# Optimization experiments

Measured on AMD Instinct MI355X. Metric: run time of the kernel, lower is better.

Reference implementation:

```python
import jax, jax.numpy as jnp
import numpy as np

QMIN, QMAX = -128.0, 127.0

@jax.custom_vjp
def ste_round(x):
    return jnp.round(x)

def _ste_fwd(x):
    return jnp.round(x), None

def _ste_bwd(_, g):
    return (g,)

ste_round.defvjp(_ste_fwd, _ste_bwd)

def fake_quant_act(x, scale):
    # Int8 per-tensor fake quant: q = clip(round(x/s)) * s
    return jnp.clip(ste_round(x / scale), QMIN, QMAX) * scale

def fake_quant_weight(w):
    # Int8WeightPerTensorFloat: scale from max-abs statistic
    s = jnp.max(jnp.abs(w)) / QMAX
    return jnp.clip(ste_round(w / s), QMIN, QMAX) * s

def conv2d(x, w, b, pad):
    y = jax.lax.conv_general_dilated(
        x, w, window_strides=(1, 1), padding=[(pad, pad), (pad, pad)],
        dimension_numbers=('NCHW', 'OIHW', 'NCHW'))
    return y + b[None, :, None, None]

def maxpool2(x):
    return jax.lax.reduce_window(
        x, -jnp.inf, jax.lax.max, (1, 1, 2, 2), (1, 1, 2, 2), 'VALID')

def setup_inputs() -> dict:
    key = jax.random.key(0)
    ks = jax.random.split(key, 12)
    def w_init(k, shape, fan_in):
        return jax.random.normal(k, shape, jnp.float32) * (1.0 / np.sqrt(fan_in))
    inp = {
        'x': jax.random.normal(ks[0], (32, 1, 256, 256), jnp.float32),
        'w1': w_init(ks[1], (16, 1, 3, 3), 1 * 9),
        'b1': jax.random.normal(ks[2], (16,), jnp.float32) * 0.01,
        'w2': w_init(ks[3], (32, 16, 3, 3), 16 * 9),
        'b2': jax.random.normal(ks[4], (32,), jnp.float32) * 0.01,
        'w3': w_init(ks[5], (32, 32, 5, 5), 32 * 25),
        'b3': jax.random.normal(ks[6], (32,), jnp.float32) * 0.01,
        'w4': w_init(ks[7], (16, 32, 3, 3), 32 * 9),
        'b4': jax.random.normal(ks[8], (16,), jnp.float32) * 0.01,
        'wc': w_init(ks[9], (10, 16), 16),
        'bc': jax.random.normal(ks[10], (10,), jnp.float32) * 0.01,
        # 11 learned per-tensor activation scales, kept strictly positive
        'act_scales': jax.random.uniform(ks[11], (11,), jnp.float32) * 0.05 + 0.01,
    }
    return inp

def reference(x, w1, b1, w2, b2, w3, b3, w4, b4, wc, bc, act_scales):
    s = act_scales
    x = fake_quant_act(x, s[0])                                  # input_quant
    x = conv2d(x, fake_quant_weight(w1), b1, 0)                  # conv1 (3x3, p0)
    x = fake_quant_act(jax.nn.relu(x), s[1])                     # relu1
    x = fake_quant_act(x, s[2])                                  # quant1
    x = conv2d(x, fake_quant_weight(w2), b2, 1)                  # conv2 (3x3, p1)
    x = fake_quant_act(jax.nn.relu(x), s[3])                     # relu2
    x = fake_quant_act(x, s[4])                                  # quant2
    x = conv2d(x, fake_quant_weight(w3), b3, 2)                  # conv3 (5x5, p2)
    x = fake_quant_act(jax.nn.relu(x), s[5])                     # relu3
    x = fake_quant_act(x, s[6])                                  # quant3
    x = maxpool2(x)                                              # pool1
    x = fake_quant_act(x, s[7])                                  # pool1_quant
    x = conv2d(x, fake_quant_weight(w4), b4, 0)                  # conv4 (3x3, p0)
    x = fake_quant_act(jax.nn.relu(x), s[8])                     # relu4
    x = fake_quant_act(x, s[9])                                  # quant4
    x = jnp.mean(x, axis=(2, 3))                                 # global avg pool -> [B,16]
    x = fake_quant_act(x, s[10])                                 # pool_quant
    return x @ fake_quant_weight(wc).T + bc                      # classifier -> [B,10]
```

## Files before the change

### kernel.cpp

```cpp
#include <hip/hip_runtime.h>
#include <math.h>


typedef int i32x4  __attribute__((ext_vector_type(4)));
typedef int i32x16 __attribute__((ext_vector_type(16)));

__device__ __forceinline__ int quant_clip(float v) {
  float r = rintf(v);
  r = fminf(fmaxf(r, -128.0f), 127.0f);
  return (int)r;
}

__device__ __forceinline__ int pack4i8(int q0, int q1, int q2, int q3) {
  return (q0 & 255) | ((q1 & 255) << 8) | ((q2 & 255) << 16) | ((q3 & 255) << 24);
}

__global__ __launch_bounds__(256) void k_quant_weights(
    const float* __restrict__ w1, const float* __restrict__ w2,
    const float* __restrict__ w3, const float* __restrict__ w4,
    const float* __restrict__ wc, float* __restrict__ wscale,
    int* __restrict__ qw1, int* __restrict__ qw2B, int* __restrict__ qw3B,
    int* __restrict__ qw4B, int* __restrict__ qwc)
{
  __shared__ float red[256];
  __shared__ float ssh;
  const int t = blockIdx.x, tid = threadIdx.x;
  const float* src = (t == 0) ? w1 : (t == 1) ? w2 : (t == 2) ? w3 : (t == 3) ? w4 : wc;
  const int nsrc   = (t == 0) ? 144 : (t == 1) ? 4608 : (t == 2) ? 25600 : (t == 3) ? 4608 : 160;

  float m = 0.0f;
  for (int i = tid; i < nsrc; i += 256) m = fmaxf(m, fabsf(src[i]));
  red[tid] = m;
  __syncthreads();
  for (int s = 128; s > 0; s >>= 1) {
    if (tid < s) red[tid] = fmaxf(red[tid], red[tid + s]);
    __syncthreads();
  }
  if (tid == 0) { ssh = red[0] / 127.0f; wscale[t] = ssh; }
  __syncthreads();
  const float s = ssh;

  if (t == 0) {
    for (int i = tid; i < 144; i += 256) qw1[i] = quant_clip(w1[i] / s);
  } else if (t == 1) {
    for (int wi = tid; wi < 1536; wi += 256) {
      int step = wi >> 8, rem = wi & 255;
      int ln = rem >> 2, w = rem & 3;
      int oc = ln & 31, h = ln >> 5;
      int ky = step >> 1, kxp = (step & 1) * 2;
      int q[4];
      #pragma unroll
      for (int j = 0; j < 4; j++) {
        int k = h * 16 + w * 4 + j;
        int ic = k & 15, kx = kxp + (k >> 4);
        float val = (kx < 3) ? w2[((oc * 16 + ic) * 3 + ky) * 3 + kx] : 0.0f;
        q[j] = quant_clip(val / s);
      }
      qw2B[wi] = pack4i8(q[0], q[1], q[2], q[3]);
    }
  } else if (t == 2) {
    for (int wi = tid; wi < 6400; wi += 256) {
      int tap = wi >> 8, rem = wi & 255;
      int ln = rem >> 2, w = rem & 3;
      int oc = ln & 31, h = ln >> 5;
      int ky = tap / 5, kx = tap % 5;
      int q[4];
      #pragma unroll
      for (int j = 0; j < 4; j++) {
        int ic = h * 16 + w * 4 + j;
        q[j] = quant_clip(w3[((oc * 32 + ic) * 5 + ky) * 5 + kx] / s);
      }
      qw3B[wi] = pack4i8(q[0], q[1], q[2], q[3]);
    }
  } else if (t == 3) {
    for (int wi = tid; wi < 1280; wi += 256) {
      int mf = wi >> 8, rem = wi & 255;
      int ln = rem >> 2, w = rem & 3;
      int oc = ln & 15, chunk = ln >> 4;
      int tp = 2 * mf + (chunk >> 1);
      int half = chunk & 1;
      int q[4];
      #pragma unroll
      for (int j = 0; j < 4; j++) {
        float val = 0.0f;
        if (tp < 9) {
          int ky = tp / 3, kx = tp % 3;
          int ic = half * 16 + w * 4 + j;
          val = w4[((oc * 32 + ic) * 3 + ky) * 3 + kx];
        }
        q[j] = quant_clip(val / s);
      }
      qw4B[wi] = pack4i8(q[0], q[1], q[2], q[3]);
    }
  } else {
    for (int wi = tid; wi < 40; wi += 256) {
      int o = wi / 4, i4 = wi % 4;
      int q[4];
      #pragma unroll
      for (int j = 0; j < 4; j++) q[j] = quant_clip(wc[o * 16 + i4 * 4 + j] / s);
      qwc[wi] = pack4i8(q[0], q[1], q[2], q[3]);
    }
  }
}

__global__ __launch_bounds__(256) void k_quant_input(
    const float* __restrict__ x, const float* __restrict__ scales,
    int* __restrict__ q0w)
{
  int i = blockIdx.x * 256 + threadIdx.x;
  if (i >= 524288) return;
  float inv = 1.0f / scales[0];
  float4 v = ((const float4*)x)[i];
  q0w[i] = pack4i8(quant_clip(v.x * inv), quant_clip(v.y * inv),
                   quant_clip(v.z * inv), quant_clip(v.w * inv));
}

__global__ __launch_bounds__(256) void k_zero_border(int* __restrict__ a2p)
{
  int i = blockIdx.x * 256 + threadIdx.x;
  int n = i >> 11, p = i & 2047;
  int row, col;
  if (p < 1032) {
    int rb = p / 258;
    row = (rb < 2) ? rb : 254 + rb;
    col = p % 258;
  } else {
    int q = p - 1032;
    int cb = q & 3;
    col = (cb < 2) ? cb : 254 + cb;
    row = 2 + (q >> 2);
  }
  int4* dst = (int4*)(a2p + (((size_t)n * 258 + row) * 258 + col) * 8);
  dst[0] = make_int4(0, 0, 0, 0);
  dst[1] = make_int4(0, 0, 0, 0);
}

__global__ __launch_bounds__(256) void k_conv1(
    const signed char* __restrict__ q0, const int* __restrict__ qw1,
    const float* __restrict__ b1, const float* __restrict__ scales,
    const float* __restrict__ wscale, int* __restrict__ a1)
{
  __shared__ int wsh[144];
  __shared__ signed char lut[128];
  if (threadIdx.x < 144) wsh[threadIdx.x] = qw1[threadIdx.x];
  if (threadIdx.x < 128) {
    float s1 = scales[1], inv2 = 1.0f / scales[2];
    lut[threadIdx.x] =
        (signed char)(int)fminf(rintf(((float)threadIdx.x * s1) * inv2), 127.0f);
  }
  __syncthreads();

  int pix = blockIdx.x * 256 + threadIdx.x;
  const int TOT = 32 * 254 * 254;
  if (pix >= TOT) return;
  int n = pix / (254 * 254), r = pix % (254 * 254);
  int oy = r / 254, ox = r % 254;

  int av[9];
  const signed char* base = q0 + (n * 256 + oy) * 256 + ox;
  #pragma unroll
  for (int ky = 0; ky < 3; ky++)
    #pragma unroll
    for (int kx = 0; kx < 3; kx++)
      av[ky * 3 + kx] = (int)base[ky * 256 + kx];

  float inv1 = 1.0f / scales[1];
  float scl = scales[0] * wscale[0];
  int outw[4];
  #pragma unroll
  for (int g = 0; g < 4; g++) {
    int q[4];
    #pragma unroll
    for (int j = 0; j < 4; j++) {
      int oc = g * 4 + j;
      int acc = 0;
      #pragma unroll
      for (int k = 0; k < 9; k++) acc += av[k] * wsh[oc * 9 + k];
      float y = fmaf(scl, (float)acc, b1[oc]);
      int idx = (int)fminf(fmaxf(rintf(y * inv1), 0.0f), 127.0f);
      q[j] = lut[idx];
    }
    outw[g] = pack4i8(q[0], q[1], q[2], q[3]);
  }
  *(int4*)(a1 + pix * 4) = make_int4(outw[0], outw[1], outw[2], outw[3]);
}

__global__ __launch_bounds__(256) void k_conv2_mfma(
    const int* __restrict__ a1, const int* __restrict__ qw2B,
    const float* __restrict__ b2, const float* __restrict__ scales,
    const float* __restrict__ wscale, signed char* __restrict__ a2p)
{
  __shared__ signed char lut[128];
  if (threadIdx.x < 128) {
    float s3 = scales[3], inv4 = 1.0f / scales[4];
    lut[threadIdx.x] =
        (signed char)(int)fminf(rintf(((float)threadIdx.x * s3) * inv4), 127.0f);
  }
  __syncthreads();

  const int lane = threadIdx.x & 63;
  const int bid = blockIdx.x;
  const int swz = (bid & 7) * 256 + (bid >> 3);
  const int gw = swz * 4 + (threadIdx.x >> 6);

  i32x4 bw[6];
  #pragma unroll
  for (int t = 0; t < 6; t++)
    bw[t] = *(const i32x4*)(qw2B + (t * 64 + lane) * 4);

  const float inv3 = 1.0f / scales[3];
  const float scl = scales[2] * wscale[1];
  const int oc = lane & 31, h = lane >> 5, rr = lane & 31;
  const float bias = b2[oc];

  const int TILES = 32 * 254 * 8;
  #pragma unroll 1
  for (int t8 = 0; t8 < 8; t8++) {
    int tile = gw * 8 + t8;
    if (tile >= TILES) break;
    int n = tile / (254 * 8);
    int r = tile % (254 * 8);
    int y = r >> 3, X0 = (r & 7) * 32;

    i32x4 Af[6];
    #pragma unroll
    for (int ky = 0; ky < 3; ky++) {
      int iy = y + ky - 1;
      bool vy = (iy >= 0) && (iy < 254);
      int iyc = min(max(iy, 0), 253);
      #pragma unroll
      for (int kp = 0; kp < 2; kp++) {
        int ix = X0 + rr + kp * 2 + h - 1;
        bool vx = (ix >= 0) && (ix < 254);
        int ixc = min(max(ix, 0), 253);
        i32x4 a = *(const i32x4*)(a1 + ((n * 254 + iyc) * 254 + ixc) * 4);
        bool v = vy && vx;
        i32x4 z;
        z[0] = v ? a[0] : 0; z[1] = v ? a[1] : 0;
        z[2] = v ? a[2] : 0; z[3] = v ? a[3] : 0;
        Af[ky * 2 + kp] = z;
      }
    }

    i32x16 acc0, acc1;
    #pragma unroll
    for (int z = 0; z < 16; z++) { acc0[z] = 0; acc1[z] = 0; }
    #pragma unroll
    for (int ky = 0; ky < 3; ky++) {
      acc0 = __builtin_amdgcn_mfma_i32_32x32x32_i8(Af[ky * 2 + 0], bw[ky * 2 + 0], acc0, 0, 0, 0);
      acc1 = __builtin_amdgcn_mfma_i32_32x32x32_i8(Af[ky * 2 + 1], bw[ky * 2 + 1], acc1, 0, 0, 0);
    }

    #pragma unroll
    for (int q = 0; q < 4; q++) {
      #pragma unroll
      for (int j = 0; j < 4; j++) {
        int row = j + 8 * q + 4 * h;
        int x = X0 + row;
        int accv = acc0[q * 4 + j] + acc1[q * 4 + j];
        float yv = fmaf(scl, (float)accv, bias);
        int idx = (int)fminf(fmaxf(rintf(yv * inv3), 0.0f), 127.0f);
        if (x < 254)
          a2p[((size_t)(n * 258 + (y + 2)) * 258 + (x + 2)) * 32 + oc] =
              lut[idx];
      }
    }
  }
}

__global__ __launch_bounds__(256, 4) void k_conv3pool_mfma(
    const signed char* __restrict__ a2p, const int* __restrict__ qw3B,
    const float* __restrict__ b3, const float* __restrict__ scales,
    const float* __restrict__ wscale, signed char* __restrict__ a3p)
{
  __shared__ int bsh[6400];
  __shared__ signed char lut56[128];
  __shared__ signed char lut67[128];
  {
    const int tid = threadIdx.x;
    for (int i = tid; i < 6400; i += 256) bsh[i] = qw3B[i];
    if (tid < 128) {
      float s5 = scales[5], s6 = scales[6];
      float inv6 = 1.0f / s6, inv7 = 1.0f / scales[7];
      lut56[tid] = (signed char)(int)fminf(rintf(((float)tid * s5) * inv6), 127.0f);
      lut67[tid] = (signed char)(int)fminf(rintf(((float)tid * s6) * inv7), 127.0f);
    }
  }
  __syncthreads();

  const int lane = threadIdx.x & 63;
  const int bid = blockIdx.x;
  const int swz = (bid & 7) * 256 + (bid >> 3);
  const int gw = swz * 4 + (threadIdx.x >> 6);

  const float inv5 = 1.0f / scales[5];
  const float scl = scales[4] * wscale[2];
  const int oc = lane & 31, h = lane >> 5;
  const float bias = b3[oc];

  const int rr = lane & 31;
  const int pp = rr >> 2, dy = (rr >> 1) & 1, dx = rr & 1;

  const int TILES = 32 * 127 * 16;
  #pragma unroll 1
  for (int t8 = 0; t8 < 8; t8++) {
    int tile = gw * 8 + t8;
    if (tile >= TILES) break;
    int n = tile / (127 * 16);
    int r = tile % (127 * 16);
    int Y = r >> 4, X0 = (r & 15) * 8;

    int py = 2 * Y + dy;
    int px = 2 * (X0 + pp) + dx;
    px = min(px, 253);
    const signed char* abase = a2p + ((size_t)(n * 258 + py) * 258 + px) * 32 + h * 16;

    i32x16 acc0, acc1;
    #pragma unroll
    for (int z = 0; z < 16; z++) { acc0[z] = 0; acc1[z] = 0; }

    i32x4 A0[5], A1[5];
    #pragma unroll
    for (int kx = 0; kx < 5; kx++)
      A0[kx] = *(const i32x4*)(abase + kx * 32);

    #pragma unroll
    for (int ky = 0; ky < 5; ky++) {
      if (ky < 4) {
        const signed char* rbn = abase + (ky + 1) * (258 * 32);
        #pragma unroll
        for (int kx = 0; kx < 5; kx++)
          A1[kx] = *(const i32x4*)(rbn + kx * 32);
      }
      #pragma unroll
      for (int kx = 0; kx < 5; kx++) {
        int tap = ky * 5 + kx;
        i32x4 b = *(const i32x4*)&bsh[(tap * 64 + lane) * 4];
        if (tap & 1)
          acc1 = __builtin_amdgcn_mfma_i32_32x32x32_i8(A0[kx], b, acc1, 0, 0, 0);
        else
          acc0 = __builtin_amdgcn_mfma_i32_32x32x32_i8(A0[kx], b, acc0, 0, 0, 0);
      }
      if (ky < 4) {
        #pragma unroll
        for (int kx = 0; kx < 5; kx++) A0[kx] = A1[kx];
      }
    }

    #pragma unroll
    for (int q = 0; q < 4; q++) {
      int b = 2 * q + h;
      int X = X0 + b;
      int a0 = acc0[q * 4 + 0] + acc1[q * 4 + 0];
      int a1v = acc0[q * 4 + 1] + acc1[q * 4 + 1];
      int a2 = acc0[q * 4 + 2] + acc1[q * 4 + 2];
      int a3 = acc0[q * 4 + 3] + acc1[q * 4 + 3];
      int am = max(max(a0, a1v), max(a2, a3));
      float yv = fmaf(scl, (float)am, bias);
      int r1 = (int)fminf(fmaxf(rintf(yv * inv5), 0.0f), 127.0f);
      int r2 = lut56[r1];
      int r3 = lut67[r2];
      if (X < 127)
        a3p[((size_t)(n * 127 + Y) * 127 + X) * 32 + oc] = (signed char)r3;
    }
  }
}

__global__ __launch_bounds__(256) void k_conv4_mfma(
    const signed char* __restrict__ a3p, const int* __restrict__ qw4B,
    const float* __restrict__ b4, const float* __restrict__ scales,
    const float* __restrict__ wscale, signed char* __restrict__ a4b)
{
  __shared__ signed char lut[128];
  if (threadIdx.x < 128) {
    float s8 = scales[8], inv9 = 1.0f / scales[9];
    lut[threadIdx.x] =
        (signed char)(int)fminf(rintf(((float)threadIdx.x * s8) * inv9), 127.0f);
  }
  __syncthreads();

  const int lane = threadIdx.x & 63;
  const int bid = blockIdx.x;
  const int swz = (bid & 7) * 256 + (bid >> 3);
  const int gw = swz * 4 + (threadIdx.x >> 6);

  i32x4 bw[5];
  #pragma unroll
  for (int t = 0; t < 5; t++)
    bw[t] = *(const i32x4*)(qw4B + (t * 64 + lane) * 4);

  const int chunk = lane >> 4;
  int offB[5];
  #pragma unroll
  for (int mf = 0; mf < 5; mf++) {
    int tp = 2 * mf + (chunk >> 1);
    if (tp > 8) tp = 8;
    int ky = tp / 3, kx = tp % 3;
    offB[mf] = (ky * 127 + kx) * 32 + (chunk & 1) * 16;
  }

  const float inv8 = 1.0f / scales[8];
  const float scl = scales[7] * wscale[3];
  const int oc = lane & 15;
  const float bias = b4[oc];
  const int arow = lane & 15;

  const int TILES = 32 * 125 * 8;
  #pragma unroll 1
  for (int t4 = 0; t4 < 4; t4++) {
    int tile = gw * 4 + t4;
    if (tile >= TILES) break;
    int n = tile / 1000;
    int r = tile % 1000;
    int y = r >> 3, X0 = (r & 7) * 16;

    const signed char* base =
        a3p + ((size_t)n * 16129 + (size_t)y * 127 + (X0 + arow)) * 32;

    i32x4 Af[5];
    #pragma unroll
    for (int mf = 0; mf < 5; mf++)
      Af[mf] = *(const i32x4*)(base + offB[mf]);

    i32x4 acc;
    acc[0] = 0; acc[1] = 0; acc[2] = 0; acc[3] = 0;
    #pragma unroll
    for (int mf = 0; mf < 5; mf++)
      acc = __builtin_amdgcn_mfma_i32_16x16x64_i8(Af[mf], bw[mf], acc, 0, 0, 0);

    #pragma unroll
    for (int j = 0; j < 4; j++) {
      int x = X0 + chunk * 4 + j;
      float yv = fmaf(scl, (float)acc[j], bias);
      int idx = (int)fminf(fmaxf(rintf(yv * inv8), 0.0f), 127.0f);
      if (x < 125)
        a4b[((size_t)(n * 125 + y) * 125 + x) * 16 + oc] = lut[idx];
    }
  }
}

__global__ __launch_bounds__(256) void k_gap_stage(
    const int* __restrict__ a4, int* __restrict__ gap_acc)
{
  int img = blockIdx.x >> 4, chunk = blockIdx.x & 15;
  int tid = threadIdx.x, lane = tid & 63;
  int p0 = chunk * 977, p1 = min(p0 + 977, 15625);

  int loc[16];
  #pragma unroll
  for (int i = 0; i < 16; i++) loc[i] = 0;
  for (int p = p0 + tid; p < p1; p += 256) {
    int4 v = *(const int4*)(a4 + (img * 15625 + p) * 4);
    int w[4] = {v.x, v.y, v.z, v.w};
    #pragma unroll
    for (int wi = 0; wi < 4; wi++)
      #pragma unroll
      for (int j = 0; j < 4; j++)
        loc[wi * 4 + j] += (int)(signed char)(w[wi] >> (8 * j));
  }
  #pragma unroll
  for (int c = 0; c < 16; c++) {
    #pragma unroll
    for (int off = 32; off > 0; off >>= 1)
      loc[c] += __shfl_down(loc[c], off);
  }
  if (lane == 0) {
    #pragma unroll
    for (int c = 0; c < 16; c++) atomicAdd(&gap_acc[img * 16 + c], loc[c]);
  }
}

__global__ __launch_bounds__(64) void k_fc(
    const int* __restrict__ gap_acc, const int* __restrict__ qwc,
    const float* __restrict__ bc, const float* __restrict__ scales,
    const float* __restrict__ wscale, float* __restrict__ out)
{
  __shared__ int sq[16];
  int n = blockIdx.x, tid = threadIdx.x;
  if (tid < 16) {
    int s = gap_acc[n * 16 + tid];
    float v = scales[9] * (float)s / 15625.0f;
    float r = fminf(fmaxf(rintf(v / scales[10]), -128.0f), 127.0f);
    sq[tid] = (int)r;
  }
  __syncthreads();
  if (tid < 10) {
    int acc = 0;
    #pragma unroll
    for (int k4 = 0; k4 < 4; k4++) {
      int wv = qwc[tid * 4 + k4];
      #pragma unroll
      for (int j = 0; j < 4; j++)
        acc += sq[k4 * 4 + j] * (int)(signed char)(wv >> (8 * j));
    }
    out[n * 10 + tid] = fmaf(scales[10] * wscale[4], (float)acc, bc[tid]);
  }
}

extern "C" void kernel_launch(void* const* d_in, const int* in_sizes, int n_in,
                              void* d_out, int out_size, void* d_ws, size_t ws_size,
                              hipStream_t stream) {
  const float* x  = (const float*)d_in[0];
  const float* w1 = (const float*)d_in[1];
  const float* b1 = (const float*)d_in[2];
  const float* w2 = (const float*)d_in[3];
  const float* b2 = (const float*)d_in[4];
  const float* w3 = (const float*)d_in[5];
  const float* b3 = (const float*)d_in[6];
  const float* w4 = (const float*)d_in[7];
  const float* b4 = (const float*)d_in[8];
  const float* wc = (const float*)d_in[9];
  const float* bc = (const float*)d_in[10];
  const float* sc = (const float*)d_in[11];

  char* ws = (char*)d_ws;
  float* wscale = (float*)(ws + 0);
  int* qw1  = (int*)(ws + 64);
  int* qw2B = (int*)(ws + 1024);
  int* qw3B = (int*)(ws + 8192);
  int* qw4B = (int*)(ws + 36864);
  int* qwc  = (int*)(ws + 43008);
  int* gap_acc = (int*)(ws + 49152);
  signed char* a2p = (signed char*)(ws + 65536);
  int*  q0  = (int*)(ws + 65536);
  int*  a4  = (int*)(ws + 65536);
  int*  a1  = (int*)(ws + 68227072);
  signed char* a3p = (signed char*)(ws + 68227072);
  float* out = (float*)d_out;

  hipMemsetAsync(gap_acc, 0, 2048, stream);
  k_quant_weights<<<5, 256, 0, stream>>>(w1, w2, w3, w4, wc, wscale,
                                         qw1, qw2B, qw3B, qw4B, qwc);
  k_quant_input<<<2048, 256, 0, stream>>>(x, sc, q0);
  k_conv1<<<8065, 256, 0, stream>>>((const signed char*)q0, qw1, b1, sc, wscale, a1);
  k_zero_border<<<256, 256, 0, stream>>>((int*)a2p);
  k_conv2_mfma<<<2048, 256, 0, stream>>>(a1, qw2B, b2, sc, wscale, a2p);
  k_conv3pool_mfma<<<2048, 256, 0, stream>>>(a2p, qw3B, b3, sc, wscale, a3p);
  k_conv4_mfma<<<2048, 256, 0, stream>>>(a3p, qw4B, b4, sc, wscale,
                                         (signed char*)a4);
  k_gap_stage<<<512, 256, 0, stream>>>(a4, gap_acc);
  k_fc<<<32, 64, 0, stream>>>(gap_acc, qwc, bc, sc, wscale, out);
}
```

Baseline: 291.8 us.

## Stage conv3 input rows in LDS and compute two pooled rows per wave

The conv3+maxpool kernel now assigns each block a fixed image/column-group/row-quarter and stages 8 input rows × 68 columns of the padded activation into shared memory per iteration, instead of each wave loading its 5×5 window directly from global memory. Each wave computes two pooled output rows at once, reusing loaded row fragments across both accumulators via a rotating register buffer so each B fragment feeds two MFMAs. This cuts redundant global loads of overlapping input rows. The cost is about 17KB more LDS, extra barriers per iteration, and a lower occupancy hint (3 blocks per CU instead of 4).

```diff
diff --git a/kernel.cpp b/kernel.cpp
--- a/kernel.cpp
+++ b/kernel.cpp
@@ -268,17 +268,42 @@
   }
 }
 
-__global__ __launch_bounds__(256, 4) void k_conv3pool_mfma(
+__global__ __launch_bounds__(256, 3) void k_conv3pool_mfma(
     const signed char* __restrict__ a2p, const int* __restrict__ qw3B,
     const float* __restrict__ b3, const float* __restrict__ scales,
     const float* __restrict__ wscale, signed char* __restrict__ a3p)
 {
+  __shared__ __align__(16) signed char ash[8 * 2176];
   __shared__ int bsh[6400];
   __shared__ signed char lut56[128];
   __shared__ signed char lut67[128];
+
+  const int tid = threadIdx.x;
+  const int lane = tid & 63;
+  const int w = tid >> 6;
+
+  const int bid = blockIdx.x;
+  const int swz = (bid & 7) * 256 + (bid >> 3);
+  const int n  = swz >> 6;
+  const int Xg = (swz >> 4) & 3;
+  const int Yq = swz & 15;
+  const int c0 = 64 * Xg;
+
+  const int oc = lane & 31, h = lane >> 5;
+  const int rr = lane & 31;
+  const int pp = rr >> 2, dy = (rr >> 1) & 1, dx = rr & 1;
+  const int xl = 8 * w + pp;
+  const int colb = (2 * xl + dx) * 32 + h * 16;
+  const int X0w = 32 * Xg + 8 * w;
+
+  const float inv5 = 1.0f / scales[5];
+  const float scl = scales[4] * wscale[2];
+  const float bias = b3[oc];
+
   {
-    const int tid = threadIdx.x;
-    for (int i = tid; i < 6400; i += 256) bsh[i] = qw3B[i];
+    const int4* srcB = (const int4*)qw3B;
+    int4* dstB = (int4*)bsh;
+    for (int i = tid; i < 1600; i += 256) dstB[i] = srcB[i];
     if (tid < 128) {
       float s5 = scales[5], s6 = scales[6];
       float inv6 = 1.0f / s6, inv7 = 1.0f / scales[7];
@@ -286,82 +311,80 @@
       lut67[tid] = (signed char)(int)fminf(rintf(((float)tid * s6) * inv7), 127.0f);
     }
   }
-  __syncthreads();
-
-  const int lane = threadIdx.x & 63;
-  const int bid = blockIdx.x;
-  const int swz = (bid & 7) * 256 + (bid >> 3);
-  const int gw = swz * 4 + (threadIdx.x >> 6);
-
-  const float inv5 = 1.0f / scales[5];
-  const float scl = scales[4] * wscale[2];
-  const int oc = lane & 31, h = lane >> 5;
-  const float bias = b3[oc];
-
-  const int rr = lane & 31;
-  const int pp = rr >> 2, dy = (rr >> 1) & 1, dx = rr & 1;
-
-  const int TILES = 32 * 127 * 16;
+
   #pragma unroll 1
-  for (int t8 = 0; t8 < 8; t8++) {
-    int tile = gw * 8 + t8;
-    if (tile >= TILES) break;
-    int n = tile / (127 * 16);
-    int r = tile % (127 * 16);
-    int Y = r >> 4, X0 = (r & 15) * 8;
-
-    int py = 2 * Y + dy;
-    int px = 2 * (X0 + pp) + dx;
-    px = min(px, 253);
-    const signed char* abase = a2p + ((size_t)(n * 258 + py) * 258 + px) * 32 + h * 16;
+  for (int it = 0; it < 4; ++it) {
+    const int Yp = 4 * Yq + it;
+    const int r0 = 4 * Yp;
+
+    __syncthreads();
+    for (int ci = tid; ci < 1088; ci += 256) {
+      int row = ci / 136;
+      int cr = ci - row * 136;
+      int col = cr >> 1, half = cr & 1;
+      int gr = min(r0 + row, 257);
+      int gc = min(c0 + col, 257);
+      const int4* srcA = (const int4*)(a2p +
+          (((size_t)n * 258 + gr) * 258 + gc) * 32 + half * 16);
+      *(int4*)(&ash[row * 2176 + cr * 16]) = *srcA;
+    }
+    __syncthreads();
 
     i32x16 acc0, acc1;
     #pragma unroll
     for (int z = 0; z < 16; z++) { acc0[z] = 0; acc1[z] = 0; }
 
-    i32x4 A0[5], A1[5];
-    #pragma unroll
-    for (int kx = 0; kx < 5; kx++)
-      A0[kx] = *(const i32x4*)(abase + kx * 32);
-
-    #pragma unroll
-    for (int ky = 0; ky < 5; ky++) {
-      if (ky < 4) {
-        const signed char* rbn = abase + (ky + 1) * (258 * 32);
-        #pragma unroll
-        for (int kx = 0; kx < 5; kx++)
-          A1[kx] = *(const i32x4*)(rbn + kx * 32);
+    i32x4 F0[5], F1[5], F2[5], F3[5];
+
+#define LOAD_ROW(F, J)                                                   \
+    {                                                                    \
+      const signed char* rbase = &ash[(dy + (J)) * 2176 + colb];         \
+      _Pragma("unroll")                                                  \
+      for (int kx = 0; kx < 5; kx++)                                     \
+        F[kx] = *(const i32x4*)(rbase + kx * 32);                        \
+    }
+#define STEP(KY, RA, RB)                                                 \
+    {                                                                    \
+      _Pragma("unroll")                                                  \
+      for (int kx = 0; kx < 5; kx++) {                                   \
+        i32x4 bfrag = *(const i32x4*)&bsh[(((KY) * 5 + kx) * 64 + lane) * 4]; \
+        acc0 = __builtin_amdgcn_mfma_i32_32x32x32_i8(RA[kx], bfrag, acc0, 0, 0, 0); \
+        acc1 = __builtin_amdgcn_mfma_i32_32x32x32_i8(RB[kx], bfrag, acc1, 0, 0, 0); \
+      }                                                                  \
+    }
+
+    LOAD_ROW(F0, 0) LOAD_ROW(F1, 1) LOAD_ROW(F2, 2)
+    LOAD_ROW(F3, 3) STEP(0, F0, F2)
+    LOAD_ROW(F0, 4) STEP(1, F1, F3)
+    LOAD_ROW(F1, 5) STEP(2, F2, F0)
+    LOAD_ROW(F2, 6) STEP(3, F3, F1)
+    STEP(4, F0, F2)
+#undef LOAD_ROW
+#undef STEP
+
+    #pragma unroll
+    for (int ty = 0; ty < 2; ty++) {
+      int Y = 2 * Yp + ty;
+      #pragma unroll
+      for (int q = 0; q < 4; q++) {
+        int b = 2 * q + h;
+        int X = X0w + b;
+        int a0, a1v, a2, a3;
+        if (ty == 0) {
+          a0 = acc0[q * 4 + 0]; a1v = acc0[q * 4 + 1];
+          a2 = acc0[q * 4 + 2]; a3 = acc0[q * 4 + 3];
+        } else {
+          a0 = acc1[q * 4 + 0]; a1v = acc1[q * 4 + 1];
+          a2 = acc1[q * 4 + 2]; a3 = acc1[q * 4 + 3];
+        }
+        int am = max(max(a0, a1v), max(a2, a3));
+        float yv = fmaf(scl, (float)am, bias);
+        int r1 = (int)fminf(fmaxf(rintf(yv * inv5), 0.0f), 127.0f);
+        int r2 = lut56[r1];
+        int r3 = lut67[r2];
+        if (X < 127 && Y < 127)
+          a3p[((size_t)(n * 127 + Y) * 127 + X) * 32 + oc] = (signed char)r3;
       }
-      #pragma unroll
-      for (int kx = 0; kx < 5; kx++) {
-        int tap = ky * 5 + kx;
-        i32x4 b = *(const i32x4*)&bsh[(tap * 64 + lane) * 4];
-        if (tap & 1)
-          acc1 = __builtin_amdgcn_mfma_i32_32x32x32_i8(A0[kx], b, acc1, 0, 0, 0);
-        else
-          acc0 = __builtin_amdgcn_mfma_i32_32x32x32_i8(A0[kx], b, acc0, 0, 0, 0);
-      }
-      if (ky < 4) {
-        #pragma unroll
-        for (int kx = 0; kx < 5; kx++) A0[kx] = A1[kx];
-      }
-    }
-
-    #pragma unroll
-    for (int q = 0; q < 4; q++) {
-      int b = 2 * q + h;
-      int X = X0 + b;
-      int a0 = acc0[q * 4 + 0] + acc1[q * 4 + 0];
-      int a1v = acc0[q * 4 + 1] + acc1[q * 4 + 1];
-      int a2 = acc0[q * 4 + 2] + acc1[q * 4 + 2];
-      int a3 = acc0[q * 4 + 3] + acc1[q * 4 + 3];
-      int am = max(max(a0, a1v), max(a2, a3));
-      float yv = fmaf(scl, (float)am, bias);
-      int r1 = (int)fminf(fmaxf(rintf(yv * inv5), 0.0f), 127.0f);
-      int r2 = lut56[r1];
-      int r3 = lut67[r2];
-      if (X < 127)
-        a3p[((size_t)(n * 127 + Y) * 127 + X) * 32 + oc] = (signed char)r3;
     }
   }
 }
```

New measurement: 279.1 us. -4.4%, faster.
